# Performance work log

Hardware: AMD Instinct MI355X
Metric: run time of the kernel (lower is better)

## Reference

```python
import jax, jax.numpy as jnp
import numpy as np

H = 16
D_MODEL = 1024
D_K = D_MODEL // H  # 64, must equal embeddim


def setup_inputs() -> dict:
    key = jax.random.key(0)
    ks = jax.random.split(key, 20)
    B, S, D = 4, 1024, D_MODEL
    s = 0.02
    inp = {
        'query': jax.random.normal(ks[0], (B, S, D), jnp.float32),
        'key':   jax.random.normal(ks[1], (B, S, D), jnp.float32),
        'value': jax.random.normal(ks[2], (B, S, D), jnp.float32),
        'mask':  jnp.ones((B, S, S), jnp.int32),
        # four d_model x d_model projections (q, k, v, out)
        'wq': jax.random.normal(ks[3], (D, D), jnp.float32) * s, 'bq': jnp.zeros((D,), jnp.float32),
        'wk': jax.random.normal(ks[4], (D, D), jnp.float32) * s, 'bk': jnp.zeros((D,), jnp.float32),
        'wv': jax.random.normal(ks[5], (D, D), jnp.float32) * s, 'bv': jnp.zeros((D,), jnp.float32),
        'wo': jax.random.normal(ks[6], (D, D), jnp.float32) * s, 'bo': jnp.zeros((D,), jnp.float32),
        # per-head (embeddim=64) linears
        'spatial_w': jax.random.normal(ks[7], (D_K, D_K), jnp.float32) * s, 'spatial_b': jnp.zeros((D_K,), jnp.float32),
        'qproj_w':   jax.random.normal(ks[8], (D_K, D_K), jnp.float32) * s, 'qproj_b':   jnp.zeros((D_K,), jnp.float32),
        'kproj_w':   jax.random.normal(ks[9], (D_K, D_K), jnp.float32) * s, 'kproj_b':   jnp.zeros((D_K,), jnp.float32),
        'vlin_w':    jax.random.normal(ks[10], (D_K, D_K), jnp.float32) * s, 'vlin_b':    jnp.zeros((D_K,), jnp.float32),
        # channel_linear: Linear(1, 64)
        'chan_w': jax.random.normal(ks[11], (1, D_K), jnp.float32) * s, 'chan_b': jnp.zeros((D_K,), jnp.float32),
    }
    return inp


def reference(query, key, value, mask,
              wq, bq, wk, bk, wv, bv, wo, bo,
              spatial_w, spatial_b, qproj_w, qproj_b,
              kproj_w, kproj_b, vlin_w, vlin_b, chan_w, chan_b):
    B, S, D = query.shape
    # project and split heads -> [B, H, S, D_K]
    def heads(x, w, b):
        return (x @ w + b).reshape(B, S, H, D_K).transpose(0, 2, 1, 3)
    q = heads(query, wq, bq)
    k = heads(key, wk, bk)
    v = heads(value, wv, bv)

    q = jax.nn.elu(q @ spatial_w + spatial_b)
    q_refine = q @ qproj_w + qproj_b
    # channel gate: mean over channels -> Linear(1,64) -> matmul with raw key
    alpha = q_refine.mean(-1, keepdims=True) @ chan_w + chan_b        # [B,H,S,64]
    gate = jax.nn.sigmoid(jnp.einsum('bhqe,bhke->bhqk', alpha, k))    # [B,H,S,S]

    k2 = jax.nn.elu(k @ kproj_w + kproj_b)
    scores = jnp.einsum('bhqe,bhke->bhqk', q, k2) / jnp.sqrt(jnp.asarray(D_K, q.dtype))
    scores = scores * gate
    scores = jnp.where(mask[:, None] == 0, jnp.asarray(-1e9, scores.dtype), scores)
    p_attn = jax.nn.softmax(scores, axis=-1)

    v2 = jax.nn.elu(v @ vlin_w + vlin_b)
    x = jnp.einsum('bhqk,bhke->bhqe', p_attn, v2)                     # [B,H,S,64]
    x = x.transpose(0, 2, 1, 3).reshape(B, S, H * D_K)
    return x @ wo + bo
```

## Files before the change

kernel.cpp:

```cpp
#include <hip/hip_runtime.h>
#include <math.h>

#define D_MODEL 1024
#define NH 16
#define DK 64
#define S_LEN 1024
#define BATCH 4
#define MROWS (BATCH * S_LEN)

typedef short bf16x8 __attribute__((ext_vector_type(8)));
typedef float f32x4 __attribute__((ext_vector_type(4)));
typedef unsigned short u16;

__device__ __forceinline__ float elu1(float x) {
    return x > 0.f ? x : (expf(x) - 1.f);
}

__device__ __forceinline__ u16 f2bf(float f) {
    union { float f; unsigned u; } v; v.f = f;
    unsigned u = v.u;
    return (u16)((u + 0x7fffu + ((u >> 16) & 1u)) >> 16);
}

__device__ __forceinline__ unsigned pack2(float a, float b) {
    union { float f; unsigned u; } ua, ub; ua.f = a; ub.f = b;
    return ((ua.u + 0x8000u) >> 16) | ((ub.u + 0x8000u) & 0xffff0000u);
}

__device__ __forceinline__ void async16(const void* g, void* l) {
    __builtin_amdgcn_global_load_lds(
        (const __attribute__((address_space(1))) unsigned int*)g,
        (__attribute__((address_space(3))) unsigned int*)l,
        16, 0, 0);
}

__global__ __launch_bounds__(256) void cast_wt(
    const float* __restrict__ wq, const float* __restrict__ wk,
    const float* __restrict__ wv, const float* __restrict__ wo,
    u16* __restrict__ WT)
{
    __shared__ float T[64][65];
    const int z = blockIdx.z;
    const float* W = (z == 0) ? wq : ((z == 1) ? wk : ((z == 2) ? wv : wo));
    u16* O = WT + (size_t)z * D_MODEL * D_MODEL;
    const int tid = threadIdx.x;
    const int k0 = blockIdx.y * 64, n0 = blockIdx.x * 64;
    const int r = tid >> 4, c4 = (tid & 15) * 4;
    #pragma unroll
    for (int p = 0; p < 4; p++) {
        float4 v = *(const float4*)&W[(size_t)(k0 + r + p * 16) * D_MODEL + n0 + c4];
        T[r + p * 16][c4 + 0] = v.x; T[r + p * 16][c4 + 1] = v.y;
        T[r + p * 16][c4 + 2] = v.z; T[r + p * 16][c4 + 3] = v.w;
    }
    __syncthreads();
    #pragma unroll
    for (int p = 0; p < 4; p++) {
        const int i = r + p * 16;
        ushort4 o4;
        o4.x = f2bf(T[c4 + 0][i]); o4.y = f2bf(T[c4 + 1][i]);
        o4.z = f2bf(T[c4 + 2][i]); o4.w = f2bf(T[c4 + 3][i]);
        *(ushort4*)&O[(size_t)(n0 + i) * D_MODEL + k0 + c4] = o4;
    }
}

__global__ __launch_bounds__(256) void proj_fused(
    const float* __restrict__ Xq, const float* __restrict__ Xk, const float* __restrict__ Xv,
    const u16* __restrict__ WTq, const u16* __restrict__ WTk, const u16* __restrict__ WTv,
    const float* __restrict__ bq, const float* __restrict__ bk, const float* __restrict__ bv,
    const float* __restrict__ spatial_w, const float* __restrict__ spatial_b,
    const float* __restrict__ qproj_w, const float* __restrict__ qproj_b,
    const float* __restrict__ kproj_w, const float* __restrict__ kproj_b,
    const float* __restrict__ vlin_w, const float* __restrict__ vlin_b,
    const float* __restrict__ chan_w, const float* __restrict__ chan_b,
    u16* __restrict__ Qh, u16* __restrict__ K2, u16* __restrict__ V2t,
    float* __restrict__ mB, float* __restrict__ uB, float* __restrict__ vB)
{
    __shared__ __align__(16) u16 smem[10752];
    __shared__ float auxA[64];
    __shared__ float auxS;

    u16* As = smem;
    u16* Bs = smem + 4096;
    u16* W2t = smem + 6144;

    const int z = blockIdx.z;
    const float* X = (z == 0) ? Xq : ((z == 1) ? Xk : Xv);
    const u16* WT = (z == 0) ? WTq : ((z == 1) ? WTk : WTv);
    const float* B1 = (z == 0) ? bq : ((z == 1) ? bk : bv);
    const float* W2 = (z == 0) ? spatial_w : ((z == 1) ? kproj_w : vlin_w);
    const float* B2 = (z == 0) ? spatial_b : ((z == 1) ? kproj_b : vlin_b);

    const int tid = threadIdx.x;
    const int wave = tid >> 6, lane = tid & 63;
    const int col = lane & 15, quad = lane >> 4;
    const int r0 = blockIdx.x * 128;
    const int hh = blockIdx.y;
    const int n0 = hh * 64;

    #pragma unroll
    for (int p = 0; p < 4; p++) {
        int idx = p * 256 + tid;
        int f = idx >> 4, e4 = (idx & 15) * 4;
        float4 w4 = *(const float4*)&W2[f * 64 + e4];
        W2t[(e4 + 0) * 72 + f] = f2bf(w4.x);
        W2t[(e4 + 1) * 72 + f] = f2bf(w4.y);
        W2t[(e4 + 2) * 72 + f] = f2bf(w4.z);
        W2t[(e4 + 3) * 72 + f] = f2bf(w4.w);
    }
    if (z == 0) {
        {
            int row = tid >> 2, part = tid & 3;
            float s = 0.f;
            for (int e = part * 16; e < part * 16 + 16; e++) s += qproj_w[row * 64 + e];
            s += __shfl_xor(s, 1);
            s += __shfl_xor(s, 2);
            if (part == 0) auxA[row] = s * (1.f / 64.f);
        }
        if (tid < 64) {
            float s = qproj_b[tid];
            #pragma unroll
            for (int m = 1; m < 64; m <<= 1) s += __shfl_xor(s, m);
            if (tid == 0) auxS = s * (1.f / 64.f);
        }
    }

    const int arow = tid >> 1, ahalf = tid & 1;
    const float* aptr = X + (size_t)(r0 + arow) * D_MODEL + ahalf * 16;
    u16* adst = As + arow * 32 + ahalf * 16;

    const u16* bp = WT + (size_t)(n0 + wave * 16 + (lane >> 2)) * D_MODEL + (lane & 3) * 8;
    u16* bdst = Bs + wave * 16 * 32;

    f32x4 acc[2][4];
    #pragma unroll
    for (int i = 0; i < 2; i++)
        #pragma unroll
        for (int j = 0; j < 4; j++)
            acc[i][j] = (f32x4){0.f, 0.f, 0.f, 0.f};

    float4 fr[4];
    #pragma unroll
    for (int i = 0; i < 4; i++) fr[i] = *(const float4*)(aptr + i * 4);

    for (int k0 = 0; k0 < D_MODEL; k0 += 32) {
        if (k0) __syncthreads();
        async16(bp + k0, bdst);
        {
            uint4 q0, q1;
            q0.x = pack2(fr[0].x, fr[0].y); q0.y = pack2(fr[0].z, fr[0].w);
            q0.z = pack2(fr[1].x, fr[1].y); q0.w = pack2(fr[1].z, fr[1].w);
            q1.x = pack2(fr[2].x, fr[2].y); q1.y = pack2(fr[2].z, fr[2].w);
            q1.z = pack2(fr[3].x, fr[3].y); q1.w = pack2(fr[3].z, fr[3].w);
            *(uint4*)adst = q0;
            *(uint4*)(adst + 8) = q1;
        }
        if (k0 + 32 < D_MODEL) {
            const float* ap = aptr + k0 + 32;
            #pragma unroll
            for (int i = 0; i < 4; i++) fr[i] = *(const float4*)(ap + i * 4);
        }
        __syncthreads();
        const u16* Abase = As + (wave * 32 + col) * 32 + quad * 8;
        const u16* Bbase = Bs + col * 32 + quad * 8;
        bf16x8 af[2], bfr[4];
        #pragma unroll
        for (int mi = 0; mi < 2; mi++) af[mi] = *(const bf16x8*)(Abase + mi * 512);
        #pragma unroll
        for (int ni = 0; ni < 4; ni++) bfr[ni] = *(const bf16x8*)(Bbase + ni * 512);
        #pragma unroll
        for (int mi = 0; mi < 2; mi++)
            #pragma unroll
            for (int ni = 0; ni < 4; ni++)
                acc[mi][ni] = __builtin_amdgcn_mfma_f32_16x16x32_bf16(af[mi], bfr[ni], acc[mi][ni], 0, 0, 0);
    }

    float b1v[4];
    #pragma unroll
    for (int ni = 0; ni < 4; ni++) b1v[ni] = B1[n0 + ni * 16 + col];

    const int rbase = r0 + wave * 32;
    const int b = r0 >> 10;
    const int s0 = (r0 & 1023) + wave * 32;
    const size_t svecbase = ((size_t)b * NH + hh) * S_LEN;

    if (z == 1) {
        float cw[4], cb[4];
        #pragma unroll
        for (int ni = 0; ni < 4; ni++) { cw[ni] = chan_w[ni * 16 + col]; cb[ni] = chan_b[ni * 16 + col]; }
        #pragma unroll
        for (int mi = 0; mi < 2; mi++)
            #pragma unroll
            for (int r = 0; r < 4; r++) {
                float su = 0.f, sv = 0.f;
                #pragma unroll
                for (int ni = 0; ni < 4; ni++) {
                    float p = acc[mi][ni][r] + b1v[ni];
                    su += p * cw[ni];
                    sv += p * cb[ni];
                }
                su += __shfl_xor(su, 1); su += __shfl_xor(su, 2);
                su += __shfl_xor(su, 4); su += __shfl_xor(su, 8);
                sv += __shfl_xor(sv, 1); sv += __shfl_xor(sv, 2);
                sv += __shfl_xor(sv, 4); sv += __shfl_xor(sv, 8);
                if (col == 0) {
                    const size_t idx = svecbase + s0 + mi * 16 + quad * 4 + r;
                    uB[idx] = su;
                    vB[idx] = sv;
                }
            }
    }

    __syncthreads();

    u16* Pchunk = smem + wave * 1536;
    bf16x8 bf2r[4][2];
    #pragma unroll
    for (int ni = 0; ni < 4; ni++) {
        bf2r[ni][0] = *(const bf16x8*)&W2t[(ni * 16 + col) * 72 + quad * 8];
        bf2r[ni][1] = *(const bf16x8*)&W2t[(ni * 16 + col) * 72 + 32 + quad * 8];
    }
    float qs[2][4][4];
    #pragma unroll
    for (int mi = 0; mi < 2; mi++) {
        #pragma unroll
        for (int ni = 0; ni < 4; ni++)
            #pragma unroll
            for (int r = 0; r < 4; r++)
                Pchunk[(quad * 4 + r) * 72 + ni * 16 + col] = f2bf(acc[mi][ni][r] + b1v[ni]);
        __builtin_amdgcn_s_waitcnt(0xc07f);
        bf16x8 a0 = *(const bf16x8*)&Pchunk[col * 72 + quad * 8];
        bf16x8 a1 = *(const bf16x8*)&Pchunk[col * 72 + 32 + quad * 8];
        __builtin_amdgcn_s_waitcnt(0xc07f);
        #pragma unroll
        for (int ni = 0; ni < 4; ni++) {
            f32x4 c = (f32x4){0.f, 0.f, 0.f, 0.f};
            c = __builtin_amdgcn_mfma_f32_16x16x32_bf16(a0, bf2r[ni][0], c, 0, 0, 0);
            c = __builtin_amdgcn_mfma_f32_16x16x32_bf16(a1, bf2r[ni][1], c, 0, 0, 0);
            const float bb = B2[ni * 16 + col];
            #pragma unroll
            for (int r = 0; r < 4; r++) qs[mi][ni][r] = elu1(c[r] + bb);
        }
    }

    if (z == 0) {
        float aw[4];
        #pragma unroll
        for (int ni = 0; ni < 4; ni++) aw[ni] = auxA[ni * 16 + col];
        #pragma unroll
        for (int mi = 0; mi < 2; mi++)
            #pragma unroll
            for (int r = 0; r < 4; r++) {
                float pm = 0.f;
                #pragma unroll
                for (int ni = 0; ni < 4; ni++) pm += qs[mi][ni][r] * aw[ni];
                pm += __shfl_xor(pm, 1); pm += __shfl_xor(pm, 2);
                pm += __shfl_xor(pm, 4); pm += __shfl_xor(pm, 8);
                if (col == 0)
                    mB[svecbase + s0 + mi * 16 + quad * 4 + r] = pm + auxS;
            }
        #pragma unroll
        for (int mi = 0; mi < 2; mi++)
            #pragma unroll
            for (int ni = 0; ni < 4; ni++)
                #pragma unroll
                for (int r = 0; r < 4; r++)
                    Qh[(size_t)(rbase + mi * 16 + quad * 4 + r) * D_MODEL
                       + n0 + ni * 16 + col] = f2bf(qs[mi][ni][r] * 0.125f);
    } else if (z == 1) {
        #pragma unroll
        for (int mi = 0; mi < 2; mi++)
            #pragma unroll
            for (int ni = 0; ni < 4; ni++)
                #pragma unroll
                for (int r = 0; r < 4; r++)
                    K2[(size_t)(rbase + mi * 16 + quad * 4 + r) * D_MODEL
                       + n0 + ni * 16 + col] = f2bf(qs[mi][ni][r]);
    } else {
        u16* Tb = W2t;
        __syncthreads();
        #pragma unroll
        for (int p = 0; p < 2; p++) {
            if ((wave >> 1) == p) {
                const int sloc = (wave & 1) * 32;
                #pragma unroll
                for (int mi = 0; mi < 2; mi++)
                    #pragma unroll
                    for (int ni = 0; ni < 4; ni++)
                        #pragma unroll
                        for (int r = 0; r < 4; r++)
                            Tb[(ni * 16 + col) * 72 + sloc + mi * 16 + quad * 4 + r] =
                                f2bf(qs[mi][ni][r]);
            }
            __syncthreads();
            {
                const int d = tid >> 2, seg = tid & 3;
                u16* dst = V2t + (((size_t)b * NH + hh) * DK + d) * S_LEN
                         + (r0 & 1023) + p * 64 + seg * 16;
                *(uint4*)dst = *(const uint4*)&Tb[d * 72 + seg * 16];
                *(uint4*)(dst + 8) = *(const uint4*)&Tb[d * 72 + seg * 16 + 8];
            }
            if (p == 0) __syncthreads();
        }
    }
}

__global__ __launch_bounds__(256) void attn_mfma(
    const u16* __restrict__ Qh, const u16* __restrict__ K2h, const u16* __restrict__ V2t,
    const float* __restrict__ Mq, const float* __restrict__ Uk, const float* __restrict__ Vk,
    const int* __restrict__ mask, u16* __restrict__ X)
{
    __shared__ u16 K2s[2][64][72];
    __shared__ u16 V2s[2][64][72];
    __shared__ u16 Ps[4][16][72];

    const int tid = threadIdx.x;
    const int wave = tid >> 6, lane = tid & 63;
    const int col = lane & 15, quad = lane >> 4;
    const int b = blockIdx.z, h = blockIdx.y;
    const int q0 = blockIdx.x * 64;
    const size_t hb = ((size_t)(b * NH + h)) * S_LEN * DK;
    const size_t sb = ((size_t)(b * NH + h)) * S_LEN;

    bf16x8 qf0, qf1;
    {
        const u16* qp = Qh + (size_t)(b * S_LEN + q0 + wave * 16 + col) * D_MODEL + h * 64 + quad * 8;
        qf0 = *(const bf16x8*)qp;
        qf1 = *(const bf16x8*)(qp + 32);
    }
    float mqv[4];
    #pragma unroll
    for (int r = 0; r < 4; r++)
        mqv[r] = Mq[sb + q0 + wave * 16 + quad * 4 + r];

    const int srow = tid >> 2, sseg = tid & 3;
    const u16* ksrc = K2h + (size_t)(b * S_LEN + srow) * D_MODEL + h * 64 + sseg * 16;
    const u16* vsrc = V2t + hb + (size_t)srow * S_LEN + sseg * 16;
    const int* mrow = mask + (size_t)b * S_LEN * S_LEN
                    + (size_t)(q0 + wave * 16 + quad * 4) * S_LEN + col;

    uint4 ka = *(const uint4*)(ksrc);
    uint4 kb = *(const uint4*)(ksrc + 8);
    uint4 va = *(const uint4*)(vsrc);
    uint4 vb = *(const uint4*)(vsrc + 8);
    float ku[4], kv[4];
    int mk[4][4];
    #pragma unroll
    for (int nb = 0; nb < 4; nb++) {
        ku[nb] = Uk[sb + nb * 16 + col];
        kv[nb] = Vk[sb + nb * 16 + col];
        #pragma unroll
        for (int r = 0; r < 4; r++) mk[nb][r] = mrow[(size_t)r * S_LEN + nb * 16];
    }

    float psum[4] = {0.f, 0.f, 0.f, 0.f};
    f32x4 o[4];
    #pragma unroll
    for (int nb = 0; nb < 4; nb++) o[nb] = (f32x4){0.f, 0.f, 0.f, 0.f};

    for (int t = 0; t < 16; t++) {
        const int bsel = t & 1;
        *(uint4*)&K2s[bsel][srow][sseg * 16]     = ka;
        *(uint4*)&K2s[bsel][srow][sseg * 16 + 8] = kb;
        *(uint4*)&V2s[bsel][srow][sseg * 16]     = va;
        *(uint4*)&V2s[bsel][srow][sseg * 16 + 8] = vb;
        __syncthreads();

        float kun[4], kvn[4];
        int mkn[4][4];
        if (t < 15) {
            const int k1 = (t + 1) * 64;
            const u16* ks = ksrc + (size_t)k1 * D_MODEL;
            const u16* vs = vsrc + k1;
            ka = *(const uint4*)(ks);
            kb = *(const uint4*)(ks + 8);
            va = *(const uint4*)(vs);
            vb = *(const uint4*)(vs + 8);
            #pragma unroll
            for (int nb = 0; nb < 4; nb++) {
                kun[nb] = Uk[sb + k1 + nb * 16 + col];
                kvn[nb] = Vk[sb + k1 + nb * 16 + col];
                #pragma unroll
                for (int r = 0; r < 4; r++)
                    mkn[nb][r] = mrow[k1 + (size_t)r * S_LEN + nb * 16];
            }
        }

        f32x4 sc[4];
        #pragma unroll
        for (int nb = 0; nb < 4; nb++) {
            bf16x8 b0 = *(const bf16x8*)&K2s[bsel][nb * 16 + col][quad * 8];
            bf16x8 b1 = *(const bf16x8*)&K2s[bsel][nb * 16 + col][32 + quad * 8];
            f32x4 c = (f32x4){0.f, 0.f, 0.f, 0.f};
            c = __builtin_amdgcn_mfma_f32_16x16x32_bf16(qf0, b0, c, 0, 0, 0);
            c = __builtin_amdgcn_mfma_f32_16x16x32_bf16(qf1, b1, c, 0, 0, 0);
            sc[nb] = c;
        }

        #pragma unroll
        for (int nb = 0; nb < 4; nb++) {
            #pragma unroll
            for (int r = 0; r < 4; r++) {
                float g = 1.f / (1.f + __expf(-(mqv[r] * ku[nb] + kv[nb])));
                float sv = sc[nb][r] * g;
                sv = mk[nb][r] ? sv : -30.f;
                float p = __expf(sv);
                psum[r] += p;
                Ps[wave][quad * 4 + r][nb * 16 + col] = f2bf(p);
            }
        }
        __builtin_amdgcn_s_waitcnt(0xc07f);
        bf16x8 a0 = *(const bf16x8*)&Ps[wave][col][quad * 8];
        bf16x8 a1 = *(const bf16x8*)&Ps[wave][col][32 + quad * 8];

        #pragma unroll
        for (int nb = 0; nb < 4; nb++) {
            bf16x8 b0 = *(const bf16x8*)&V2s[bsel][nb * 16 + col][quad * 8];
            bf16x8 b1 = *(const bf16x8*)&V2s[bsel][nb * 16 + col][32 + quad * 8];
            o[nb] = __builtin_amdgcn_mfma_f32_16x16x32_bf16(a0, b0, o[nb], 0, 0, 0);
            o[nb] = __builtin_amdgcn_mfma_f32_16x16x32_bf16(a1, b1, o[nb], 0, 0, 0);
        }

        if (t < 15) {
            #pragma unroll
            for (int nb = 0; nb < 4; nb++) {
                ku[nb] = kun[nb]; kv[nb] = kvn[nb];
                #pragma unroll
                for (int r = 0; r < 4; r++) mk[nb][r] = mkn[nb][r];
            }
        }
    }

    #pragma unroll
    for (int r = 0; r < 4; r++) {
        float t = psum[r];
        t += __shfl_xor(t, 1);
        t += __shfl_xor(t, 2);
        t += __shfl_xor(t, 4);
        t += __shfl_xor(t, 8);
        float inv = 1.f / t;
        u16* xp = X + (size_t)(b * S_LEN + q0 + wave * 16 + quad * 4 + r) * D_MODEL + h * 64 + col;
        #pragma unroll
        for (int nb = 0; nb < 4; nb++)
            xp[nb * 16] = f2bf(o[nb][r] * inv);
    }
}

__global__ __launch_bounds__(256) void out_gemm(
    const u16* __restrict__ A, const u16* __restrict__ WT,
    const float* __restrict__ bias, float* __restrict__ C)
{
    __shared__ u16 As[64 * 32];
    __shared__ u16 Bs[64 * 32];

    const int tid = threadIdx.x;
    const int wave = tid >> 6, lane = tid & 63;
    const int col = lane & 15, quad = lane >> 4;
    const int r0 = blockIdx.x * 64, n0 = blockIdx.y * 64;

    const u16* ap = A + (size_t)(r0 + wave * 16 + (lane >> 2)) * D_MODEL + (lane & 3) * 8;
    const u16* bp = WT + (size_t)(n0 + wave * 16 + (lane >> 2)) * D_MODEL + (lane & 3) * 8;
    u16* adst = As + wave * 16 * 32;
    u16* bdst = Bs + wave * 16 * 32;

    f32x4 acc[4];
    #pragma unroll
    for (int j = 0; j < 4; j++) acc[j] = (f32x4){0.f, 0.f, 0.f, 0.f};

    for (int k0 = 0; k0 < D_MODEL; k0 += 32) {
        if (k0) __syncthreads();
        async16(ap + k0, adst);
        async16(bp + k0, bdst);
        __syncthreads();
        const u16* Ab = As + (wave * 16 + col) * 32 + quad * 8;
        const u16* Bb = Bs + col * 32 + quad * 8;
        bf16x8 af = *(const bf16x8*)Ab;
        bf16x8 bfr[4];
        #pragma unroll
        for (int ni = 0; ni < 4; ni++) bfr[ni] = *(const bf16x8*)(Bb + ni * 512);
        #pragma unroll
        for (int ni = 0; ni < 4; ni++)
            acc[ni] = __builtin_amdgcn_mfma_f32_16x16x32_bf16(af, bfr[ni], acc[ni], 0, 0, 0);
    }

    #pragma unroll
    for (int ni = 0; ni < 4; ni++) {
        const int gr = r0 + wave * 16 + quad * 4;
        const int gc = n0 + ni * 16 + col;
        const float bb = bias[gc];
        #pragma unroll
        for (int r = 0; r < 4; r++)
            C[(size_t)(gr + r) * D_MODEL + gc] = acc[ni][r] + bb;
    }
}

extern "C" void kernel_launch(void* const* d_in, const int* in_sizes, int n_in,
                              void* d_out, int out_size, void* d_ws, size_t ws_size,
                              hipStream_t stream) {
    (void)in_sizes; (void)n_in; (void)out_size; (void)ws_size;
    const float* query = (const float*)d_in[0];
    const float* key_  = (const float*)d_in[1];
    const float* value = (const float*)d_in[2];
    const int*   mask  = (const int*)d_in[3];
    const float* wq = (const float*)d_in[4];  const float* bq = (const float*)d_in[5];
    const float* wk = (const float*)d_in[6];  const float* bk = (const float*)d_in[7];
    const float* wv = (const float*)d_in[8];  const float* bv = (const float*)d_in[9];
    const float* wo = (const float*)d_in[10]; const float* bo = (const float*)d_in[11];
    const float* spatial_w = (const float*)d_in[12]; const float* spatial_b = (const float*)d_in[13];
    const float* qproj_w   = (const float*)d_in[14]; const float* qproj_b   = (const float*)d_in[15];
    const float* kproj_w   = (const float*)d_in[16]; const float* kproj_b   = (const float*)d_in[17];
    const float* vlin_w    = (const float*)d_in[18]; const float* vlin_b    = (const float*)d_in[19];
    const float* chan_w    = (const float*)d_in[20]; const float* chan_b    = (const float*)d_in[21];
    float* out = (float*)d_out;

    char* ws = (char*)d_ws;
    u16* Qh  = (u16*)ws;
    u16* K2  = (u16*)(ws + ((size_t)8  << 20));
    u16* Xb  = (u16*)(ws + ((size_t)16 << 20));
    u16* WT  = (u16*)(ws + ((size_t)24 << 20));
    u16* V2t = (u16*)(ws + ((size_t)32 << 20));
    float* mB = (float*)(ws + ((size_t)40 << 20));
    float* uB = mB + (size_t)BATCH * NH * S_LEN;
    float* vB = uB + (size_t)BATCH * NH * S_LEN;
    const size_t WSZ = (size_t)D_MODEL * D_MODEL;

    cast_wt<<<dim3(16, 16, 4), 256, 0, stream>>>(wq, wk, wv, wo, WT);
    proj_fused<<<dim3(32, 16, 3), 256, 0, stream>>>(query, key_, value,
        WT, WT + WSZ, WT + 2 * WSZ, bq, bk, bv,
        spatial_w, spatial_b, qproj_w, qproj_b, kproj_w, kproj_b,
        vlin_w, vlin_b, chan_w, chan_b,
        Qh, K2, V2t, mB, uB, vB);
    attn_mfma<<<dim3(S_LEN / 64, NH, BATCH), 256, 0, stream>>>(Qh, K2, V2t, mB, uB, vB, mask, Xb);
    out_gemm<<<dim3(64, 16), 256, 0, stream>>>(Xb, WT + 3 * WSZ, bo, out);
}
```

Baseline: 316.7 us.

## Pre-cast activations to bf16 and swizzle LDS tiles in projection/output GEMMs

Adds a separate kernel that converts the q/k/v fp32 inputs to bf16 once, so the projection GEMM can stream its A tiles with async global-to-LDS loads instead of loading fp32 into registers and packing them in the loop. The LDS layout of A and B tiles in both the projection and output GEMMs is XOR-swizzled to reduce bank conflicts on the fragment reads. This costs an extra kernel launch and a full extra read/write of the activations (about 24MB of bf16 written, 48MB read). The rounding also changes from round-half-up to round-to-nearest-even.

```diff
diff --git a/kernel.cpp b/kernel.cpp
--- a/kernel.cpp
+++ b/kernel.cpp
@@ -20,11 +20,6 @@
     union { float f; unsigned u; } v; v.f = f;
     unsigned u = v.u;
     return (u16)((u + 0x7fffu + ((u >> 16) & 1u)) >> 16);
-}
-
-__device__ __forceinline__ unsigned pack2(float a, float b) {
-    union { float f; unsigned u; } ua, ub; ua.f = a; ub.f = b;
-    return ((ua.u + 0x8000u) >> 16) | ((ub.u + 0x8000u) & 0xffff0000u);
 }
 
 __device__ __forceinline__ void async16(const void* g, void* l) {
@@ -63,8 +58,25 @@
     }
 }
 
+__global__ __launch_bounds__(256) void cast_x(
+    const float* __restrict__ Xq, const float* __restrict__ Xk,
+    const float* __restrict__ Xv, u16* __restrict__ Xb)
+{
+    const int z = blockIdx.y;
+    const float* X = (z == 0) ? Xq : ((z == 1) ? Xk : Xv);
+    u16* O = Xb + (size_t)z * MROWS * D_MODEL;
+    const size_t i = ((size_t)blockIdx.x * 256 + threadIdx.x) * 8;
+    float4 a = *(const float4*)&X[i];
+    float4 b = *(const float4*)&X[i + 4];
+    ushort4 o0, o1;
+    o0.x = f2bf(a.x); o0.y = f2bf(a.y); o0.z = f2bf(a.z); o0.w = f2bf(a.w);
+    o1.x = f2bf(b.x); o1.y = f2bf(b.y); o1.z = f2bf(b.z); o1.w = f2bf(b.w);
+    *(ushort4*)&O[i] = o0;
+    *(ushort4*)&O[i + 4] = o1;
+}
+
 __global__ __launch_bounds__(256) void proj_fused(
-    const float* __restrict__ Xq, const float* __restrict__ Xk, const float* __restrict__ Xv,
+    const u16* __restrict__ Xq, const u16* __restrict__ Xk, const u16* __restrict__ Xv,
     const u16* __restrict__ WTq, const u16* __restrict__ WTk, const u16* __restrict__ WTv,
     const float* __restrict__ bq, const float* __restrict__ bk, const float* __restrict__ bv,
     const float* __restrict__ spatial_w, const float* __restrict__ spatial_b,
@@ -84,7 +96,7 @@
     u16* W2t = smem + 6144;
 
     const int z = blockIdx.z;
-    const float* X = (z == 0) ? Xq : ((z == 1) ? Xk : Xv);
+    const u16* X = (z == 0) ? Xq : ((z == 1) ? Xk : Xv);
     const u16* WT = (z == 0) ? WTq : ((z == 1) ? WTk : WTv);
     const float* B1 = (z == 0) ? bq : ((z == 1) ? bk : bv);
     const float* W2 = (z == 0) ? spatial_w : ((z == 1) ? kproj_w : vlin_w);
@@ -124,11 +136,13 @@
         }
     }
 
-    const int arow = tid >> 1, ahalf = tid & 1;
-    const float* aptr = X + (size_t)(r0 + arow) * D_MODEL + ahalf * 16;
-    u16* adst = As + arow * 32 + ahalf * 16;
-
-    const u16* bp = WT + (size_t)(n0 + wave * 16 + (lane >> 2)) * D_MODEL + (lane & 3) * 8;
+    const int srow = lane >> 2;
+    const int sg = ((lane & 3) ^ ((lane >> 3) & 3)) * 8;
+
+    const u16* ap = X + (size_t)(r0 + wave * 32 + srow) * D_MODEL + sg;
+    u16* adst0 = As + (wave * 32) * 32;
+    u16* adst1 = As + (wave * 32 + 16) * 32;
+    const u16* bp = WT + (size_t)(n0 + wave * 16 + srow) * D_MODEL + sg;
     u16* bdst = Bs + wave * 16 * 32;
 
     f32x4 acc[2][4];
@@ -138,30 +152,16 @@
         for (int j = 0; j < 4; j++)
             acc[i][j] = (f32x4){0.f, 0.f, 0.f, 0.f};
 
-    float4 fr[4];
-    #pragma unroll
-    for (int i = 0; i < 4; i++) fr[i] = *(const float4*)(aptr + i * 4);
+    const int gsw = (quad ^ ((col >> 1) & 3)) * 8;
 
     for (int k0 = 0; k0 < D_MODEL; k0 += 32) {
         if (k0) __syncthreads();
+        async16(ap + k0, adst0);
+        async16(ap + (size_t)16 * D_MODEL + k0, adst1);
         async16(bp + k0, bdst);
-        {
-            uint4 q0, q1;
-            q0.x = pack2(fr[0].x, fr[0].y); q0.y = pack2(fr[0].z, fr[0].w);
-            q0.z = pack2(fr[1].x, fr[1].y); q0.w = pack2(fr[1].z, fr[1].w);
-            q1.x = pack2(fr[2].x, fr[2].y); q1.y = pack2(fr[2].z, fr[2].w);
-            q1.z = pack2(fr[3].x, fr[3].y); q1.w = pack2(fr[3].z, fr[3].w);
-            *(uint4*)adst = q0;
-            *(uint4*)(adst + 8) = q1;
-        }
-        if (k0 + 32 < D_MODEL) {
-            const float* ap = aptr + k0 + 32;
-            #pragma unroll
-            for (int i = 0; i < 4; i++) fr[i] = *(const float4*)(ap + i * 4);
-        }
         __syncthreads();
-        const u16* Abase = As + (wave * 32 + col) * 32 + quad * 8;
-        const u16* Bbase = Bs + col * 32 + quad * 8;
+        const u16* Abase = As + (wave * 32 + col) * 32 + gsw;
+        const u16* Bbase = Bs + col * 32 + gsw;
         bf16x8 af[2], bfr[4];
         #pragma unroll
         for (int mi = 0; mi < 2; mi++) af[mi] = *(const bf16x8*)(Abase + mi * 512);
@@ -457,22 +457,25 @@
     const int col = lane & 15, quad = lane >> 4;
     const int r0 = blockIdx.x * 64, n0 = blockIdx.y * 64;
 
-    const u16* ap = A + (size_t)(r0 + wave * 16 + (lane >> 2)) * D_MODEL + (lane & 3) * 8;
-    const u16* bp = WT + (size_t)(n0 + wave * 16 + (lane >> 2)) * D_MODEL + (lane & 3) * 8;
+    const int sg = ((lane & 3) ^ ((lane >> 3) & 3)) * 8;
+    const u16* ap = A + (size_t)(r0 + wave * 16 + (lane >> 2)) * D_MODEL + sg;
+    const u16* bp = WT + (size_t)(n0 + wave * 16 + (lane >> 2)) * D_MODEL + sg;
     u16* adst = As + wave * 16 * 32;
     u16* bdst = Bs + wave * 16 * 32;
 
     f32x4 acc[4];
     #pragma unroll
     for (int j = 0; j < 4; j++) acc[j] = (f32x4){0.f, 0.f, 0.f, 0.f};
+
+    const int gsw = (quad ^ ((col >> 1) & 3)) * 8;
 
     for (int k0 = 0; k0 < D_MODEL; k0 += 32) {
         if (k0) __syncthreads();
         async16(ap + k0, adst);
         async16(bp + k0, bdst);
         __syncthreads();
-        const u16* Ab = As + (wave * 16 + col) * 32 + quad * 8;
-        const u16* Bb = Bs + col * 32 + quad * 8;
+        const u16* Ab = As + (wave * 16 + col) * 32 + gsw;
+        const u16* Bb = Bs + col * 32 + gsw;
         bf16x8 af = *(const bf16x8*)Ab;
         bf16x8 bfr[4];
         #pragma unroll
@@ -521,10 +524,13 @@
     float* mB = (float*)(ws + ((size_t)40 << 20));
     float* uB = mB + (size_t)BATCH * NH * S_LEN;
     float* vB = uB + (size_t)BATCH * NH * S_LEN;
+    u16* Xbf = (u16*)(ws + ((size_t)42 << 20));
     const size_t WSZ = (size_t)D_MODEL * D_MODEL;
+    const size_t XSZ = (size_t)MROWS * D_MODEL;
 
     cast_wt<<<dim3(16, 16, 4), 256, 0, stream>>>(wq, wk, wv, wo, WT);
-    proj_fused<<<dim3(32, 16, 3), 256, 0, stream>>>(query, key_, value,
+    cast_x<<<dim3(MROWS * D_MODEL / 2048, 3), 256, 0, stream>>>(query, key_, value, Xbf);
+    proj_fused<<<dim3(32, 16, 3), 256, 0, stream>>>(Xbf, Xbf + XSZ, Xbf + 2 * XSZ,
         WT, WT + WSZ, WT + 2 * WSZ, bq, bk, bv,
         spatial_w, spatial_b, qproj_w, qproj_b, kproj_w, kproj_b,
         vlin_w, vlin_b, chan_w, chan_b,
```

After: 294.0 us. 1.08x faster.
